# Performance work log

Hardware: AMD Instinct MI355X
Metric: run time of the kernel (lower is better)

The kernel has to match this reference:

```python
import jax, jax.numpy as jnp
import numpy as np

EMBED = 512
HEADS = 64
DK = EMBED // HEADS  # == n_wires_attn == 8
NW_FFN = 8
FFN = 2048
EPS = 1e-5


def _layernorm(x, g, b):
    mu = jnp.mean(x, axis=-1, keepdims=True)
    var = jnp.var(x, axis=-1, keepdims=True)
    return (x - mu) * jax.lax.rsqrt(var + EPS) * g + b


def setup_inputs() -> dict:
    key = jax.random.key(0)
    ks = jax.random.split(key, 12)
    d = {
        "x": jax.random.normal(ks[0], (4, 1024, EMBED), dtype=jnp.float32),
        # attention quantum RX params (one per wire, shared across heads/tokens)
        "phi": jax.random.normal(ks[1], (DK,), dtype=jnp.float32) * 0.1,
        # combine_heads linear
        "Wc": jax.random.normal(ks[2], (EMBED, EMBED), dtype=jnp.float32) / np.sqrt(EMBED),
        "bc": jnp.zeros((EMBED,), dtype=jnp.float32),
        # FFN quantum RY params
        "theta": jax.random.normal(ks[3], (NW_FFN,), dtype=jnp.float32) * 0.1,
        "W1": jax.random.normal(ks[4], (NW_FFN, FFN), dtype=jnp.float32) / np.sqrt(NW_FFN),
        "b1": jnp.zeros((FFN,), dtype=jnp.float32),
        "W2": jax.random.normal(ks[5], (FFN, EMBED), dtype=jnp.float32) / np.sqrt(FFN),
        "b2": jnp.zeros((EMBED,), dtype=jnp.float32),
        "g1": jnp.ones((EMBED,), dtype=jnp.float32),
        "be1": jnp.zeros((EMBED,), dtype=jnp.float32),
        "g2": jnp.ones((EMBED,), dtype=jnp.float32),
        "be2": jnp.zeros((EMBED,), dtype=jnp.float32),
    }
    return d


def reference(x, phi, Wc, bc, theta, W1, b1, W2, b2, g1, be1, g2, be2):
    B, S, E = x.shape
    # --- quantum attention projections ---
    # Per head-row of DK features: RX(x_i) encoder then trainable RX(phi_i),
    xh = x.reshape(B, S, HEADS, DK)
    qkv = jnp.cos(xh + phi)                     # [B,S,H,DK]
    qkv = jnp.transpose(qkv, (0, 2, 1, 3))      # [B,H,S,DK]
    scores = jnp.einsum('bhqd,bhkd->bhqk', qkv, qkv) / jnp.sqrt(jnp.float32(DK))
    attn = jax.nn.softmax(scores, axis=-1)
    out = jnp.einsum('bhqk,bhkd->bhqd', attn, qkv)
    out = jnp.transpose(out, (0, 2, 1, 3)).reshape(B, S, E)
    attn_out = out @ Wc.T if False else out @ Wc + bc  # combine_heads linear
    x1 = _layernorm(x + attn_out, g1, be1)
    # --- quantum FFN: RX(x_i) then trainable RY(theta_i) -> <Z> = cos(x_i)*cos(theta_i)
    qout = jnp.cos(x1[..., :NW_FFN]) * jnp.cos(theta)   # [B,S,NW_FFN]
    h = jax.nn.relu(qout @ W1 + b1)
    ffn_out = h @ W2 + b2
    return _layernorm(x1 + ffn_out, g2, be2)
```

## Files before the change

kernel.cpp:

```cpp
#include <hip/hip_runtime.h>
#include <hip/hip_bf16.h>
#include <math.h>

#define B 4
#define S 1024
#define E 512
#define H 64
#define DK 8
#define FFN 2048
#define BS (B*S)

#define CSCALE 0.7141879f

#if __has_builtin(__builtin_amdgcn_exp2f)
#define EXP2F(x) __builtin_amdgcn_exp2f(x)
#else
#define EXP2F(x) exp2f(x)
#endif

typedef __attribute__((ext_vector_type(8))) short short8;
typedef __attribute__((ext_vector_type(4))) float float4a;

union U8 { short8 v; unsigned u[4]; };
union F4 { float4a v; float f[4]; };

__device__ __forceinline__ unsigned short f2bf(float f) {
    unsigned u = __builtin_bit_cast(unsigned, f);
    u = (u + 0x7fffu + ((u >> 16) & 1u)) >> 16;
    return (unsigned short)u;
}
__device__ __forceinline__ float bf2f(unsigned short h) {
    return __builtin_bit_cast(float, (unsigned)h << 16);
}
__device__ __forceinline__ unsigned packbf(float a, float b) {
    return __builtin_amdgcn_perm(__builtin_bit_cast(unsigned, a),
                                 __builtin_bit_cast(unsigned, b), 0x07060302u);
}
__device__ __forceinline__ unsigned packbf_rn(float a, float b) {
    return ((unsigned)f2bf(a) << 16) | f2bf(b);
}
__device__ __forceinline__ int pidx(int k) {
    return (k & ~31) | (((k >> 2) & 3) << 3) | (((k >> 4) & 1) << 2) | (k & 3);
}

__device__ __forceinline__ void glds16(const void* g, void* l) {
    __builtin_amdgcn_global_load_lds(
        (const __attribute__((address_space(1))) void*)g,
        (__attribute__((address_space(3))) void*)l, 16, 0, 0);
}

__global__ __launch_bounds__(512) void attn_conv_kernel(const float* __restrict__ x,
                                                        const float* __restrict__ phi,
                                                        const float* __restrict__ Wc,
                                                        const float* __restrict__ W2,
                                                        const float* __restrict__ W1,
                                                        const float* __restrict__ b1,
                                                        unsigned short* __restrict__ Afrag,
                                                        unsigned short* __restrict__ W2f,
                                                        unsigned short* __restrict__ Wcf,
                                                        unsigned short* __restrict__ W1f) {
    __shared__ unsigned short kv[(S + 16) * DK];
    __shared__ unsigned short vtp[9][S + 8];
    int bid = blockIdx.x;
    int tid = threadIdx.x;
    const short8 z8 = {0,0,0,0,0,0,0,0};

    if (bid < 336) {
        int idx = bid * 512 + tid;
        if (idx < 131072) {
            int lane = idx & 63, c = idx >> 6;
            int ntile = c >> 6, kb32 = c & 63;
            int g = lane >> 4, col = lane & 15;
            int n = ntile * 16 + col, kb = kb32 * 32;
            short8 o;
            #pragma unroll
            for (int j = 0; j < 8; j++) {
                int k = kb + 16 * (j >> 2) + 4 * g + (j & 3);
                o[j] = (short)f2bf(W2[(size_t)k * 512 + n]);
            }
            *(short8*)&W2f[(size_t)idx * 8] = o;
        } else if (idx < 163840) {
            int i2 = idx - 131072;
            int lane = i2 & 63, c = i2 >> 6;
            int ntile = c >> 4, kb32 = c & 15;
            int g = lane >> 4, col = lane & 15;
            int n = ntile * 16 + col, kb = kb32 * 32;
            short8 o;
            #pragma unroll
            for (int j = 0; j < 8; j++)
                o[j] = (short)f2bf(Wc[(size_t)(kb + g * 8 + j) * 512 + n]);
            *(short8*)&Wcf[(size_t)i2 * 8] = o;
        } else {
            int i3 = idx - 163840;
            if (i3 < 2048) {
                short8 o;
                #pragma unroll
                for (int j = 0; j < 8; j++) o[j] = (short)f2bf(W1[j * FFN + i3]);
                *(short8*)&W1f[(size_t)i3 * 8] = o;
            } else if (i3 < 4096) {
                int f = i3 - 2048;
                W1f[16384 + f] = f2bf(b1[f]);
            }
        }
        return;
    }

    int abid = bid - 336;
    int head = abid >> 2, qquad = abid & 3;
    int b = head >> 6, hh = head & 63;

    float ph[DK];
    #pragma unroll
    for (int d = 0; d < DK; d++) ph[d] = phi[d];

    {
        int r2 = tid * 2;
        unsigned short vb[8][2];
        #pragma unroll
        for (int j = 0; j < 2; j++) {
            const float* xp = x + ((size_t)(b * S + r2 + j)) * E + hh * DK;
            float4 u = *(const float4*)xp;
            float4 v = *(const float4*)(xp + 4);
            float c[8] = {__cosf(u.x+ph[0]), __cosf(u.y+ph[1]), __cosf(u.z+ph[2]), __cosf(u.w+ph[3]),
                          __cosf(v.x+ph[4]), __cosf(v.y+ph[5]), __cosf(v.z+ph[6]), __cosf(v.w+ph[7])};
            U8 kr;
            kr.u[0] = packbf_rn(c[1] * CSCALE, c[0] * CSCALE);
            kr.u[1] = packbf_rn(c[3] * CSCALE, c[2] * CSCALE);
            kr.u[2] = packbf_rn(c[5] * CSCALE, c[4] * CSCALE);
            kr.u[3] = packbf_rn(c[7] * CSCALE, c[6] * CSCALE);
            *(short8*)&kv[(r2 + j) * DK] = kr.v;
            #pragma unroll
            for (int d = 0; d < 8; d++) vb[d][j] = f2bf(c[d]);
        }
        int pr = pidx(r2);
        #pragma unroll
        for (int d = 0; d < 8; d++)
            *(unsigned*)&vtp[d][pr] = (unsigned)vb[d][0] | ((unsigned)vb[d][1] << 16);
        *(unsigned*)&vtp[8][pr] = 0x3F803F80u;
    }
    if (tid < 16) *(short8*)&kv[(S + tid) * DK] = z8;
    __syncthreads();

    int w = tid >> 6, lane = tid & 63, col = lane & 15, g = lane >> 4;
    bool g0 = (g == 0);
    int q0 = qquad * 256 + w * 32;
    const float4a zc = {0.f,0.f,0.f,0.f};

    short8 aq[2];
    #pragma unroll
    for (int t = 0; t < 2; t++)
        aq[t] = g0 ? *(const short8*)&kv[(q0 + t*16 + col) * DK] : z8;

    float4a acc[2];
    acc[0] = zc; acc[1] = zc;

    int vrow = col < 8 ? col : 8;
    const unsigned short* vbase = &vtp[vrow][0];

    int off0 = g0 ? col * DK : S * DK;
    int off1 = g0 ? (16 + col) * DK : S * DK;
    int stepo = g0 ? 32 * DK : 0;

    short8 bk0 = *(const short8*)&kv[off0];
    short8 bk1 = *(const short8*)&kv[off1];
    off0 += stepo; off1 += stepo;

    for (int kb = 0; kb < S; kb += 32) {
        __builtin_amdgcn_s_setprio(1);
        float4a s00 = __builtin_amdgcn_mfma_f32_16x16x32_bf16(bk0, aq[0], zc, 0,0,0);
        float4a s01 = __builtin_amdgcn_mfma_f32_16x16x32_bf16(bk1, aq[0], zc, 0,0,0);
        float4a s10 = __builtin_amdgcn_mfma_f32_16x16x32_bf16(bk0, aq[1], zc, 0,0,0);
        float4a s11 = __builtin_amdgcn_mfma_f32_16x16x32_bf16(bk1, aq[1], zc, 0,0,0);
        __builtin_amdgcn_s_setprio(0);
        short8 vf = *(const short8*)(vbase + kb + g * 8);
        short8 nbk0 = *(const short8*)&kv[off0];
        short8 nbk1 = *(const short8*)&kv[off1];
        off0 += stepo; off1 += stepo;
        F4 S00, S01, S10, S11;
        S00.v = s00; S01.v = s01; S10.v = s10; S11.v = s11;
        float ea0 = EXP2F(S00.f[0]);
        float ea1 = EXP2F(S00.f[1]);
        float ea2 = EXP2F(S00.f[2]);
        float ea3 = EXP2F(S00.f[3]);
        float eb0 = EXP2F(S01.f[0]);
        float eb1 = EXP2F(S01.f[1]);
        float eb2 = EXP2F(S01.f[2]);
        float eb3 = EXP2F(S01.f[3]);
        float ec0 = EXP2F(S10.f[0]);
        float ec1 = EXP2F(S10.f[1]);
        float ec2 = EXP2F(S10.f[2]);
        float ec3 = EXP2F(S10.f[3]);
        float ed0 = EXP2F(S11.f[0]);
        float ed1 = EXP2F(S11.f[1]);
        float ed2 = EXP2F(S11.f[2]);
        float ed3 = EXP2F(S11.f[3]);
        U8 pf0, pf1;
        pf0.u[0] = packbf(ea1, ea0);
        pf0.u[1] = packbf(ea3, ea2);
        pf0.u[2] = packbf(eb1, eb0);
        pf0.u[3] = packbf(eb3, eb2);
        pf1.u[0] = packbf(ec1, ec0);
        pf1.u[1] = packbf(ec3, ec2);
        pf1.u[2] = packbf(ed1, ed0);
        pf1.u[3] = packbf(ed3, ed2);
        __builtin_amdgcn_s_setprio(1);
        acc[0] = __builtin_amdgcn_mfma_f32_16x16x32_bf16(vf, pf0.v, acc[0], 0,0,0);
        acc[1] = __builtin_amdgcn_mfma_f32_16x16x32_bf16(vf, pf1.v, acc[1], 0,0,0);
        __builtin_amdgcn_s_setprio(0);
        bk0 = nbk0; bk1 = nbk1;
    }
    int lp8 = ((hh & 3) * 16 + col) * 8;
    #pragma unroll
    for (int t = 0; t < 2; t++) {
        F4 a; a.v = acc[t];
        float denom = __shfl(a.f[0], 32 + col);
        float inv = __builtin_amdgcn_rcpf(denom);
        if (g < 2) {
            int chunk = (hh >> 2) * 256 + (b * 64 + qquad * 16 + w * 2 + t);
            uint2 o;
            o.x = packbf_rn(a.f[1] * inv, a.f[0] * inv);
            o.y = packbf_rn(a.f[3] * inv, a.f[2] * inv);
            *(uint2*)&Afrag[(size_t)chunk * 512 + lp8 + g * 4] = o;
        }
    }
}

__global__ __launch_bounds__(512) void combine_ln1(const unsigned short* __restrict__ Afrag,
                                                   const unsigned short* __restrict__ Wcf,
                                                   const float* __restrict__ bc,
                                                   const float* __restrict__ x,
                                                   const float* __restrict__ g1,
                                                   const float* __restrict__ be1,
                                                   float* __restrict__ x1out,
                                                   unsigned short* __restrict__ qoutbf,
                                                   const float* __restrict__ theta) {
    __shared__ unsigned short As[16 * 64 * 8];
    __shared__ unsigned short Wcs[2][2048 * 8];
    __shared__ float xout[16][516];
    int tt = blockIdx.x;
    int tid = threadIdx.x;
    int w = tid >> 6, lane = tid & 63;
    int wbase = (tid & ~63) * 8;

    #pragma unroll
    for (int r = 0; r < 2; r++) {
        const unsigned short* gsrc =
            Afrag + ((size_t)((r * 8 + w) * 256 + tt) * 64 + lane) * 8;
        glds16(gsrc, &As[r * 4096 + wbase]);
    }
    #pragma unroll
    for (int r = 0; r < 4; r++) {
        int nt = r * 8 + w;
        glds16(Wcf + ((size_t)(nt * 16 + 0) * 64 + lane) * 8, &Wcs[0][nt * 512]);
    }
    #pragma unroll
    for (int r = 0; r < 4; r++) {
        int nt = r * 8 + w;
        glds16(Wcf + ((size_t)(nt * 16 + 1) * 64 + lane) * 8, &Wcs[1][nt * 512]);
    }
    asm volatile("s_waitcnt vmcnt(4)" ::: "memory");
    __builtin_amdgcn_s_barrier();

    int col = lane & 15, g = lane >> 4;
    const float4a zc = {0.f,0.f,0.f,0.f};
    float4a acc[4];
    #pragma unroll
    for (int nt = 0; nt < 4; nt++) acc[nt] = zc;

    for (int kb32 = 0; kb32 < 16; kb32++) {
        int cur = kb32 & 1;
        short8 af = *(const short8*)&As[(kb32 * 64 + lane) * 8];
        #pragma unroll
        for (int nt = 0; nt < 4; nt++) {
            short8 bf = *(const short8*)&Wcs[cur][((w * 4 + nt) * 64 + lane) * 8];
            acc[nt] = __builtin_amdgcn_mfma_f32_16x16x32_bf16(af, bf, acc[nt], 0, 0, 0);
        }
        if (kb32 < 15) {
            asm volatile("s_waitcnt lgkmcnt(0)" ::: "memory");
            __builtin_amdgcn_s_barrier();
            if (kb32 < 14) {
                #pragma unroll
                for (int r = 0; r < 4; r++) {
                    int nt = r * 8 + w;
                    glds16(Wcf + ((size_t)(nt * 16 + kb32 + 2) * 64 + lane) * 8,
                           &Wcs[cur][nt * 512]);
                }
                asm volatile("s_waitcnt vmcnt(4)" ::: "memory");
            } else {
                asm volatile("s_waitcnt vmcnt(0)" ::: "memory");
            }
            __builtin_amdgcn_s_barrier();
        }
    }
    #pragma unroll
    for (int nt = 0; nt < 4; nt++) {
        int n = w * 64 + nt * 16 + col;
        float bb = bc[n];
        #pragma unroll
        for (int r = 0; r < 4; r++)
            xout[g * 4 + r][n] = acc[nt][r] + bb;
    }
    __syncthreads();

    int hl = lane >> 5, l = lane & 31;
    int token = w * 2 + hl;
    int e0 = l * 16;
    size_t grow = ((size_t)tt * 16 + token) * 512;
    float v[16];
    float s = 0.f, sq = 0.f;
    #pragma unroll
    for (int u = 0; u < 4; u++) {
        float4 xv = *(const float4*)&x[grow + e0 + u * 4];
        float4 pv = *(const float4*)&xout[token][e0 + u * 4];
        float a0 = xv.x + pv.x, a1 = xv.y + pv.y, a2 = xv.z + pv.z, a3 = xv.w + pv.w;
        v[u*4] = a0; v[u*4+1] = a1; v[u*4+2] = a2; v[u*4+3] = a3;
        s += a0 + a1 + a2 + a3;
        sq += a0*a0 + a1*a1 + a2*a2 + a3*a3;
    }
    #pragma unroll
    for (int off = 1; off <= 16; off <<= 1) {
        s  += __shfl_xor(s, off);
        sq += __shfl_xor(sq, off);
    }
    float mu = s * (1.f / 512.f);
    float var = sq * (1.f / 512.f) - mu * mu;
    float rstd = rsqrtf(var + 1e-5f);
    float y[16];
    #pragma unroll
    for (int u = 0; u < 4; u++) {
        float4 gv = *(const float4*)&g1[e0 + u * 4];
        float4 bv = *(const float4*)&be1[e0 + u * 4];
        y[u*4]   = (v[u*4]   - mu) * rstd * gv.x + bv.x;
        y[u*4+1] = (v[u*4+1] - mu) * rstd * gv.y + bv.y;
        y[u*4+2] = (v[u*4+2] - mu) * rstd * gv.z + bv.z;
        y[u*4+3] = (v[u*4+3] - mu) * rstd * gv.w + bv.w;
        float4 o = make_float4(y[u*4], y[u*4+1], y[u*4+2], y[u*4+3]);
        *(float4*)&x1out[grow + e0 + u * 4] = o;
    }
    if (l == 0) {
        U8 q;
        q.u[0] = packbf_rn(__cosf(y[1]) * __cosf(theta[1]), __cosf(y[0]) * __cosf(theta[0]));
        q.u[1] = packbf_rn(__cosf(y[3]) * __cosf(theta[3]), __cosf(y[2]) * __cosf(theta[2]));
        q.u[2] = packbf_rn(__cosf(y[5]) * __cosf(theta[5]), __cosf(y[4]) * __cosf(theta[4]));
        q.u[3] = packbf_rn(__cosf(y[7]) * __cosf(theta[7]), __cosf(y[6]) * __cosf(theta[6]));
        *(short8*)&qoutbf[((size_t)tt * 16 + token) * 8] = q.v;
    }
}

__global__ __launch_bounds__(256) void ffn_mfma(const unsigned short* __restrict__ qbf,
                                                const unsigned short* __restrict__ W1fg,
                                                const unsigned short* __restrict__ W2f,
                                                const float* __restrict__ b2,
                                                unsigned short* __restrict__ Cbf) {
    __shared__ unsigned short w1x[FFN * 8];
    __shared__ unsigned short b1s[FFN];
    __shared__ float accs[2][64][36];
    int tid = threadIdx.x;
    int wbase = (tid & ~63) * 8;
    #pragma unroll
    for (int r = 0; r < 8; r++)
        glds16(W1fg + (size_t)(r * 256 + tid) * 8, &w1x[r * 2048 + wbase]);
    glds16(W1fg + 16384 + (size_t)tid * 8, &b1s[wbase]);
    asm volatile("s_waitcnt vmcnt(0)" ::: "memory");
    __syncthreads();

    int w = tid >> 6, lane = tid & 63, col = lane & 15, g = lane >> 4;
    int ngw = w & 1, kh = w >> 1;
    int tb = blockIdx.x >> 2, nb = blockIdx.x & 3;
    int mw = tb * 32;
    int ntile0 = nb * 8 + ngw * 4;
    int kb32b = kh * 32;
    const short8 z8 = {0,0,0,0,0,0,0,0};
    const short8 one8 = {(short)0x3F80,0,0,0,0,0,0,0};
    const float4a zc = {0.f,0.f,0.f,0.f};

    short8 qf[2];
    #pragma unroll
    for (int t = 0; t < 2; t++)
        qf[t] = (g == 0) ? *(const short8*)&qbf[(size_t)(mw + t * 16 + col) * 8]
                         : (g == 1 ? one8 : z8);

    float4a acc[2][4];
    #pragma unroll
    for (int t = 0; t < 2; t++)
        #pragma unroll
        for (int nt = 0; nt < 4; nt++) acc[t][nt] = zc;

    const unsigned short* w2p = W2f + (size_t)ntile0 * 64 * 512 + lane * 8;

    short8 afA[4], afB[4];
    #pragma unroll
    for (int nt = 0; nt < 4; nt++)
        afA[nt] = *(const short8*)(w2p + nt * 32768 + (size_t)kb32b * 512);

#define FFN_BODY(KB32, AF)                                                        \
    {                                                                             \
        int kb = (KB32) * 32;                                                     \
        short8 w1f0, w1f1;                                                        \
        if (g == 0) {                                                             \
            w1f0 = *(const short8*)&w1x[(kb + col) * 8];                          \
            w1f1 = *(const short8*)&w1x[(kb + 16 + col) * 8];                     \
        } else if (g == 1) {                                                      \
            w1f0 = z8; w1f1 = z8;                                                 \
            w1f0[0] = (short)b1s[kb + col];                                       \
            w1f1[0] = (short)b1s[kb + 16 + col];                                  \
        } else { w1f0 = z8; w1f1 = z8; }                                          \
        _Pragma("unroll")                                                         \
        for (int t = 0; t < 2; t++) {                                             \
            float4a h0 = __builtin_amdgcn_mfma_f32_16x16x32_bf16(w1f0, qf[t], zc, 0,0,0); \
            float4a h1 = __builtin_amdgcn_mfma_f32_16x16x32_bf16(w1f1, qf[t], zc, 0,0,0); \
            F4 H0, H1; H0.v = h0; H1.v = h1;                                      \
            float e00 = fmaxf(H0.f[0], 0.f);                                      \
            float e01 = fmaxf(H0.f[1], 0.f);                                      \
            float e02 = fmaxf(H0.f[2], 0.f);                                      \
            float e03 = fmaxf(H0.f[3], 0.f);                                      \
            float e10 = fmaxf(H1.f[0], 0.f);                                      \
            float e11 = fmaxf(H1.f[1], 0.f);                                      \
            float e12 = fmaxf(H1.f[2], 0.f);                                      \
            float e13 = fmaxf(H1.f[3], 0.f);                                      \
            U8 pf;                                                                \
            pf.u[0] = packbf(e01, e00);                                           \
            pf.u[1] = packbf(e03, e02);                                           \
            pf.u[2] = packbf(e11, e10);                                           \
            pf.u[3] = packbf(e13, e12);                                           \
            _Pragma("unroll")                                                     \
            for (int nt = 0; nt < 4; nt++)                                        \
                acc[t][nt] = __builtin_amdgcn_mfma_f32_16x16x32_bf16(AF[nt], pf.v, \
                                                                     acc[t][nt], 0,0,0); \
        }                                                                         \
    }

    for (int i = 0; i < 32; i += 2) {
        int kb32 = kb32b + i;
        #pragma unroll
        for (int nt = 0; nt < 4; nt++)
            afB[nt] = *(const short8*)(w2p + nt * 32768 + (size_t)(kb32 + 1) * 512);
        FFN_BODY(kb32, afA)
        if (i + 2 < 32) {
            #pragma unroll
            for (int nt = 0; nt < 4; nt++)
                afA[nt] = *(const short8*)(w2p + nt * 32768 + (size_t)(kb32 + 2) * 512);
        }
        FFN_BODY(kb32 + 1, afB)
    }
#undef FFN_BODY

    if (kh == 1) {
        #pragma unroll
        for (int t = 0; t < 2; t++)
            #pragma unroll
            for (int nt = 0; nt < 4; nt++)
                *(float4a*)&accs[ngw][lane][(t * 4 + nt) * 4] = acc[t][nt];
    }
    __syncthreads();
    if (kh == 0) {
        #pragma unroll
        for (int t = 0; t < 2; t++)
            #pragma unroll
            for (int nt = 0; nt < 4; nt++)
                acc[t][nt] = acc[t][nt] +
                    *(const float4a*)&accs[ngw][lane][(t * 4 + nt) * 4];
        int n0 = ntile0 * 16;
        #pragma unroll
        for (int nt = 0; nt < 4; nt++) {
            float4 bb = *(const float4*)&b2[n0 + nt * 16 + 4 * g];
            #pragma unroll
            for (int t = 0; t < 2; t++) {
                F4 a; a.v = acc[t][nt];
                uint2 o;
                o.x = packbf_rn(a.f[1] + bb.y, a.f[0] + bb.x);
                o.y = packbf_rn(a.f[3] + bb.w, a.f[2] + bb.z);
                *(uint2*)&Cbf[(size_t)(mw + t * 16 + col) * 512 + n0 + nt * 16 + 4 * g] = o;
            }
        }
    }
}

__global__ __launch_bounds__(256) void ln_kernel(const float* __restrict__ a,
                                                 const unsigned short* __restrict__ r,
                                                 const float* __restrict__ g,
                                                 const float* __restrict__ be,
                                                 float* __restrict__ out) {
    int t = blockIdx.x * 4 + (threadIdx.x >> 6);
    int lane = threadIdx.x & 63;
    size_t base = (size_t)t * E;
    int e0 = lane * 8;
    float4 a0 = *(const float4*)&a[base + e0];
    float4 a1 = *(const float4*)&a[base + e0 + 4];
    uint4 rv = *(const uint4*)&r[base + e0];
    float v[8];
    v[0] = a0.x + bf2f((unsigned short)(rv.x & 0xffff));
    v[1] = a0.y + bf2f((unsigned short)(rv.x >> 16));
    v[2] = a0.z + bf2f((unsigned short)(rv.y & 0xffff));
    v[3] = a0.w + bf2f((unsigned short)(rv.y >> 16));
    v[4] = a1.x + bf2f((unsigned short)(rv.z & 0xffff));
    v[5] = a1.y + bf2f((unsigned short)(rv.z >> 16));
    v[6] = a1.z + bf2f((unsigned short)(rv.w & 0xffff));
    v[7] = a1.w + bf2f((unsigned short)(rv.w >> 16));
    float s = 0.f, sq = 0.f;
    #pragma unroll
    for (int i = 0; i < 8; i++) { s += v[i]; sq += v[i] * v[i]; }
    #pragma unroll
    for (int off = 1; off <= 32; off <<= 1) {
        s  += __shfl_xor(s, off);
        sq += __shfl_xor(sq, off);
    }
    float mu = s * (1.f / E);
    float var = sq * (1.f / E) - mu * mu;
    float rstd = rsqrtf(var + 1e-5f);
    float4 g0 = *(const float4*)&g[e0];
    float4 g1v = *(const float4*)&g[e0 + 4];
    float4 b0 = *(const float4*)&be[e0];
    float4 b1v = *(const float4*)&be[e0 + 4];
    float4 o0, o1;
    o0.x = (v[0] - mu) * rstd * g0.x + b0.x;
    o0.y = (v[1] - mu) * rstd * g0.y + b0.y;
    o0.z = (v[2] - mu) * rstd * g0.z + b0.z;
    o0.w = (v[3] - mu) * rstd * g0.w + b0.w;
    o1.x = (v[4] - mu) * rstd * g1v.x + b1v.x;
    o1.y = (v[5] - mu) * rstd * g1v.y + b1v.y;
    o1.z = (v[6] - mu) * rstd * g1v.z + b1v.z;
    o1.w = (v[7] - mu) * rstd * g1v.w + b1v.w;
    *(float4*)&out[base + e0] = o0;
    *(float4*)&out[base + e0 + 4] = o1;
}

extern "C" void kernel_launch(void* const* d_in, const int* in_sizes, int n_in,
                              void* d_out, int out_size, void* d_ws, size_t ws_size,
                              hipStream_t stream) {
    const float* x     = (const float*)d_in[0];
    const float* phi   = (const float*)d_in[1];
    const float* Wc    = (const float*)d_in[2];
    const float* bc    = (const float*)d_in[3];
    const float* theta = (const float*)d_in[4];
    const float* W1    = (const float*)d_in[5];
    const float* b1    = (const float*)d_in[6];
    const float* W2    = (const float*)d_in[7];
    const float* b2    = (const float*)d_in[8];
    const float* g1    = (const float*)d_in[9];
    const float* be1   = (const float*)d_in[10];
    const float* g2    = (const float*)d_in[11];
    const float* be2   = (const float*)d_in[12];
    float* out = (float*)d_out;

    float* ws = (float*)d_ws;
    unsigned short* Afrag  = (unsigned short*)ws;
    unsigned short* W2f    = (unsigned short*)(ws + 1048576);
    unsigned short* Wcf    = (unsigned short*)(ws + 1572864);
    unsigned short* W1f    = (unsigned short*)(ws + 1703936);
    unsigned short* qoutbf = (unsigned short*)(ws + 1736704);

    attn_conv_kernel<<<1360, 512, 0, stream>>>(x, phi, Wc, W2, W1, b1,
                                               Afrag, W2f, Wcf, W1f);
    combine_ln1<<<256, 512, 0, stream>>>(Afrag, Wcf, bc, x, g1, be1,
                                         out, qoutbf, theta);
    ffn_mfma<<<512, 256, 0, stream>>>(qoutbf, W1f, W2f, b2, Afrag);
    ln_kernel<<<1024, 256, 0, stream>>>(out, Afrag, g2, be2, out);
}
```

Measured before the change: 158.6 us.

## Load Wc and W1 fragments directly from global into registers, dropping LDS staging

The combine_ln1 kernel no longer stages Wc tiles through double-buffered shared memory with barriers. Each wave now loads its B fragments straight from global memory into registers with a two-deep software prefetch. The FFN kernel likewise drops the shared-memory copy of W1 and b1 and streams pre-padded fragments from global, with the prep kernel writing bias and zero rows in fragment form. This removes LDS traffic, barriers and shared-memory footprint, which may help occupancy. In exchange it adds redundant global/L2 reads, and the unguarded afA prefetch may read past the end on the last iteration.

```diff
diff --git a/kernel.cpp b/kernel.cpp
--- a/kernel.cpp
+++ b/kernel.cpp
@@ -99,7 +99,11 @@
                 *(short8*)&W1f[(size_t)i3 * 8] = o;
             } else if (i3 < 4096) {
                 int f = i3 - 2048;
-                W1f[16384 + f] = f2bf(b1[f]);
+                short8 o = z8;
+                o[0] = (short)f2bf(b1[f]);
+                *(short8*)&W1f[(size_t)i3 * 8] = o;
+            } else if (i3 < 4112) {
+                *(short8*)&W1f[(size_t)i3 * 8] = z8;
             }
         }
         return;
@@ -235,7 +239,6 @@
                                                    unsigned short* __restrict__ qoutbf,
                                                    const float* __restrict__ theta) {
     __shared__ unsigned short As[16 * 64 * 8];
-    __shared__ unsigned short Wcs[2][2048 * 8];
     __shared__ float xout[16][516];
     int tt = blockIdx.x;
     int tid = threadIdx.x;
@@ -248,18 +251,8 @@
             Afrag + ((size_t)((r * 8 + w) * 256 + tt) * 64 + lane) * 8;
         glds16(gsrc, &As[r * 4096 + wbase]);
     }
-    #pragma unroll
-    for (int r = 0; r < 4; r++) {
-        int nt = r * 8 + w;
-        glds16(Wcf + ((size_t)(nt * 16 + 0) * 64 + lane) * 8, &Wcs[0][nt * 512]);
-    }
-    #pragma unroll
-    for (int r = 0; r < 4; r++) {
-        int nt = r * 8 + w;
-        glds16(Wcf + ((size_t)(nt * 16 + 1) * 64 + lane) * 8, &Wcs[1][nt * 512]);
-    }
-    asm volatile("s_waitcnt vmcnt(4)" ::: "memory");
-    __builtin_amdgcn_s_barrier();
+    asm volatile("s_waitcnt vmcnt(0)" ::: "memory");
+    __syncthreads();
 
     int col = lane & 15, g = lane >> 4;
     const float4a zc = {0.f,0.f,0.f,0.f};
@@ -267,30 +260,30 @@
     #pragma unroll
     for (int nt = 0; nt < 4; nt++) acc[nt] = zc;
 
-    for (int kb32 = 0; kb32 < 16; kb32++) {
-        int cur = kb32 & 1;
+    const unsigned short* wp = Wcf + ((size_t)(w * 4096) + lane) * 8;
+
+    short8 bfA[4], bfB[4];
+    #pragma unroll
+    for (int nt = 0; nt < 4; nt++)
+        bfA[nt] = *(const short8*)(wp + nt * 8192);
+
+    for (int kb32 = 0; kb32 < 16; kb32 += 2) {
+        #pragma unroll
+        for (int nt = 0; nt < 4; nt++)
+            bfB[nt] = *(const short8*)(wp + nt * 8192 + (kb32 + 1) * 512);
         short8 af = *(const short8*)&As[(kb32 * 64 + lane) * 8];
         #pragma unroll
-        for (int nt = 0; nt < 4; nt++) {
-            short8 bf = *(const short8*)&Wcs[cur][((w * 4 + nt) * 64 + lane) * 8];
-            acc[nt] = __builtin_amdgcn_mfma_f32_16x16x32_bf16(af, bf, acc[nt], 0, 0, 0);
+        for (int nt = 0; nt < 4; nt++)
+            acc[nt] = __builtin_amdgcn_mfma_f32_16x16x32_bf16(af, bfA[nt], acc[nt], 0, 0, 0);
+        if (kb32 + 2 < 16) {
+            #pragma unroll
+            for (int nt = 0; nt < 4; nt++)
+                bfA[nt] = *(const short8*)(wp + nt * 8192 + (kb32 + 2) * 512);
         }
-        if (kb32 < 15) {
-            asm volatile("s_waitcnt lgkmcnt(0)" ::: "memory");
-            __builtin_amdgcn_s_barrier();
-            if (kb32 < 14) {
-                #pragma unroll
-                for (int r = 0; r < 4; r++) {
-                    int nt = r * 8 + w;
-                    glds16(Wcf + ((size_t)(nt * 16 + kb32 + 2) * 64 + lane) * 8,
-                           &Wcs[cur][nt * 512]);
-                }
-                asm volatile("s_waitcnt vmcnt(4)" ::: "memory");
-            } else {
-                asm volatile("s_waitcnt vmcnt(0)" ::: "memory");
-            }
-            __builtin_amdgcn_s_barrier();
-        }
+        af = *(const short8*)&As[((kb32 + 1) * 64 + lane) * 8];
+        #pragma unroll
+        for (int nt = 0; nt < 4; nt++)
+            acc[nt] = __builtin_amdgcn_mfma_f32_16x16x32_bf16(af, bfB[nt], acc[nt], 0, 0, 0);
     }
     #pragma unroll
     for (int nt = 0; nt < 4; nt++) {
@@ -352,18 +345,8 @@
                                                 const unsigned short* __restrict__ W2f,
                                                 const float* __restrict__ b2,
                                                 unsigned short* __restrict__ Cbf) {
-    __shared__ unsigned short w1x[FFN * 8];
-    __shared__ unsigned short b1s[FFN];
     __shared__ float accs[2][64][36];
     int tid = threadIdx.x;
-    int wbase = (tid & ~63) * 8;
-    #pragma unroll
-    for (int r = 0; r < 8; r++)
-        glds16(W1fg + (size_t)(r * 256 + tid) * 8, &w1x[r * 2048 + wbase]);
-    glds16(W1fg + 16384 + (size_t)tid * 8, &b1s[wbase]);
-    asm volatile("s_waitcnt vmcnt(0)" ::: "memory");
-    __syncthreads();
-
     int w = tid >> 6, lane = tid & 63, col = lane & 15, g = lane >> 4;
     int ngw = w & 1, kh = w >> 1;
     int tb = blockIdx.x >> 2, nb = blockIdx.x & 3;
@@ -387,28 +370,26 @@
         for (int nt = 0; nt < 4; nt++) acc[t][nt] = zc;
 
     const unsigned short* w2p = W2f + (size_t)ntile0 * 64 * 512 + lane * 8;
-
-    short8 afA[4], afB[4];
+    const unsigned short* w1p =
+        (g == 0) ? W1fg + (size_t)(kb32b * 32 + col) * 8 :
+        (g == 1) ? W1fg + 16384 + (size_t)(kb32b * 32 + col) * 8 :
+                   W1fg + 32768;
+    int w1step = (g < 2) ? 256 : 0;
+
+    short8 afA[4], afB[4], w1A0, w1A1, w1B0, w1B1;
     #pragma unroll
     for (int nt = 0; nt < 4; nt++)
         afA[nt] = *(const short8*)(w2p + nt * 32768 + (size_t)kb32b * 512);
-
-#define FFN_BODY(KB32, AF)                                                        \
+    w1A0 = *(const short8*)w1p;
+    w1A1 = *(const short8*)(w1p + 128);
+    w1p += w1step;
+
+#define FFN_BODY(AF, W10, W11)                                                    \
     {                                                                             \
-        int kb = (KB32) * 32;                                                     \
-        short8 w1f0, w1f1;                                                        \
-        if (g == 0) {                                                             \
-            w1f0 = *(const short8*)&w1x[(kb + col) * 8];                          \
-            w1f1 = *(const short8*)&w1x[(kb + 16 + col) * 8];                     \
-        } else if (g == 1) {                                                      \
-            w1f0 = z8; w1f1 = z8;                                                 \
-            w1f0[0] = (short)b1s[kb + col];                                       \
-            w1f1[0] = (short)b1s[kb + 16 + col];                                  \
-        } else { w1f0 = z8; w1f1 = z8; }                                          \
         _Pragma("unroll")                                                         \
         for (int t = 0; t < 2; t++) {                                             \
-            float4a h0 = __builtin_amdgcn_mfma_f32_16x16x32_bf16(w1f0, qf[t], zc, 0,0,0); \
-            float4a h1 = __builtin_amdgcn_mfma_f32_16x16x32_bf16(w1f1, qf[t], zc, 0,0,0); \
+            float4a h0 = __builtin_amdgcn_mfma_f32_16x16x32_bf16(W10, qf[t], zc, 0,0,0); \
+            float4a h1 = __builtin_amdgcn_mfma_f32_16x16x32_bf16(W11, qf[t], zc, 0,0,0); \
             F4 H0, H1; H0.v = h0; H1.v = h1;                                      \
             float e00 = fmaxf(H0.f[0], 0.f);                                      \
             float e01 = fmaxf(H0.f[1], 0.f);                                      \
@@ -435,13 +416,17 @@
         #pragma unroll
         for (int nt = 0; nt < 4; nt++)
             afB[nt] = *(const short8*)(w2p + nt * 32768 + (size_t)(kb32 + 1) * 512);
-        FFN_BODY(kb32, afA)
-        if (i + 2 < 32) {
-            #pragma unroll
-            for (int nt = 0; nt < 4; nt++)
-                afA[nt] = *(const short8*)(w2p + nt * 32768 + (size_t)(kb32 + 2) * 512);
-        }
-        FFN_BODY(kb32 + 1, afB)
+        w1B0 = *(const short8*)w1p;
+        w1B1 = *(const short8*)(w1p + 128);
+        w1p += w1step;
+        FFN_BODY(afA, w1A0, w1A1)
+        #pragma unroll
+        for (int nt = 0; nt < 4; nt++)
+            afA[nt] = *(const short8*)(w2p + nt * 32768 + (size_t)(kb32 + 2) * 512);
+        w1A0 = *(const short8*)w1p;
+        w1A1 = *(const short8*)(w1p + 128);
+        w1p += w1step;
+        FFN_BODY(afB, w1B0, w1B1)
     }
 #undef FFN_BODY
 
```

After: 155.7 us (median of 3 runs). No clear change (-1.9%).
